# Performance work log

Hardware: AMD Instinct MI355X
Metric: run time of the kernel (lower is better)

Reference implementation:

```python
import jax, jax.numpy as jnp
import numpy as np

B, SEQ, D, H, E = 4, 4096, 1024, 4096, 8
CAPACITY = 2.0  # k = int(S * capacity) token-expert slots


def setup_inputs() -> dict:
    key = jax.random.key(0)
    ks = jax.random.split(key, 5)
    x = jax.random.normal(ks[0], (B, SEQ, D), dtype=jnp.float32)
    gate_weight = jax.random.normal(ks[1], (E, D), dtype=jnp.float32) * 0.006
    expert_bias = jnp.ones((E, 1), dtype=jnp.float32)
    W1 = jax.random.normal(ks[2], (E, D, H), dtype=jnp.float32) * 0.02
    b1 = jnp.zeros((E, H), dtype=jnp.float32)
    W2 = jax.random.normal(ks[3], (E, H, D), dtype=jnp.float32) * 0.02
    b2 = jnp.zeros((E, D), dtype=jnp.float32)
    return {"x": x, "gate_weight": gate_weight, "expert_bias": expert_bias,
            "W1": W1, "b1": b1, "W2": W2, "b2": b2}


def reference(x, gate_weight, expert_bias, W1, b1, W2, b2):
    Bv, s, Dv = x.shape
    xf = x.reshape(-1, Dv)               # [S, D]
    S = xf.shape[0]
    k = int(S * CAPACITY)

    # router: bias_sigmoid -> scores[e, s] = sigmoid(x @ gate.T + bias)
    logits = jnp.einsum('sd,ed->es', xf, gate_weight) + expert_bias  # [E, S]
    scores = jax.nn.sigmoid(logits)

    # global top-k over flattened (E*S) token-expert pairs
    value, index = jax.lax.top_k(scores.reshape(-1), k)
    index_expert = index // S
    index_token = index % S

    # combine weights: gating score at selected slots, 0 elsewhere (topk indices unique)
    C = jnp.zeros((E * S,), dtype=scores.dtype).at[index].set(value).reshape(E, S)

    token_each_expert = jax.ops.segment_sum(
        jnp.ones((k,), dtype=jnp.float32), index_expert, num_segments=E) / float(k)

    # per-expert MLP, gated combine (tokens with C==0 contribute exactly 0,
    # matching the torch gather/MLP/index_add_ path)
    out = jnp.zeros_like(xf)
    for e in range(E):
        h = jax.nn.gelu(xf @ W1[e] + b1[e], approximate=True)  # [S, H]
        y = h @ W2[e] + b2[e]                                  # [S, D]
        out = out + C[e][:, None] * y

    x_out = out.reshape(Bv, s, Dv)
    return x_out, token_each_expert, jnp.ones((E,), dtype=scores.dtype)
```

## Files before the change

kernel.cpp:

```cpp
#include <hip/hip_runtime.h>
#include <hip/hip_bf16.h>
#include <cstdint>
#include <cstdio>
#include <math.h>

#define S_TOK 16384
#define E_EXP 8
#define DDIM  1024
#define HDIM  4096
#define K_SEL 32768
#define ES    131072
#define OUT_XO 16777216

#define WS_META    0x000000u
#define WS_HIST    0x000100u
#define WS_COUNTS  0x001100u
#define WS_EXOFF   0x001200u
#define WS_TIEIDX  0x001300u
#define WS_CLEAR   0x00A000u
#define WS_TOK     0x010000u
#define WS_COEF    0x090000u
#define WS_SCORES  0x110000u
#define WS_TCNT    0x190000u
#define WS_TSLOT   0x1A0000u
#define WS_XB      0x400000u
#define WS_W1T    0x2400000u
#define WS_W2T    0x6400000u
#define WS_HBUF   0xA400000u
#define WS_TOTAL  0x1A400000u
#define WS_YBUF   WS_W1T

typedef __attribute__((ext_vector_type(4))) float f32x4;
typedef __attribute__((ext_vector_type(8))) short bf16x8;

__device__ __forceinline__ void gload_lds16(const void* g, void* l) {
  __builtin_amdgcn_global_load_lds((const __attribute__((address_space(1))) void*)g,
                                   (__attribute__((address_space(3))) void*)l, 16, 0, 0);
}

__device__ __forceinline__ float gelu_f(float x) {
  float u = __builtin_fmaf(x * x * x, 0.044715f, x);
  float e = __builtin_amdgcn_exp2f(-2.302207976f * u);
  return x * __builtin_amdgcn_rcpf(1.0f + e);
}

#define ABUF0 0
#define ABUF1 32768
#define BBUF0 65536
#define BBUF1 98304
#define HALF  16384

#define PH_BAR() __builtin_amdgcn_s_barrier()
#define VMC0M()  asm volatile("s_waitcnt vmcnt(0)" ::: "memory")
#define VMCN(N)  asm volatile("s_waitcnt vmcnt(" #N ")" ::: "memory")

#define STAGE_A(DST, KE) do { \
  gload_lds16(aS00 + (KE), lds + (DST) + w * 2048); \
  gload_lds16(aS01 + (KE), lds + (DST) + w * 2048 + 1024); \
  gload_lds16(aS10 + (KE), lds + (DST) + HALF + w * 2048); \
  gload_lds16(aS11 + (KE), lds + (DST) + HALF + w * 2048 + 1024); } while (0)
#define STAGE_B(DST, KE) do { \
  gload_lds16(bS00 + (KE), lds + (DST) + w * 2048); \
  gload_lds16(bS01 + (KE), lds + (DST) + w * 2048 + 1024); \
  gload_lds16(bS10 + (KE), lds + (DST) + HALF + w * 2048); \
  gload_lds16(bS11 + (KE), lds + (DST) + HALF + w * 2048 + 1024); } while (0)

#define LDS_A03(AB) { _Pragma("unroll") for (int ii = 0; ii < 4; ii++) { \
  a03[ii][0] = *(const bf16x8*)(lds + (AB) + arow + ii * 2048 + pc0); \
  a03[ii][1] = *(const bf16x8*)(lds + (AB) + arow + ii * 2048 + pc1); } }
#define LDS_A47(AB) { _Pragma("unroll") for (int ii = 0; ii < 4; ii++) { \
  a47[ii][0] = *(const bf16x8*)(lds + (AB) + arow + (4 + ii) * 2048 + pc0); \
  a47[ii][1] = *(const bf16x8*)(lds + (AB) + arow + (4 + ii) * 2048 + pc1); } }
#define LDS_B01(BB) { _Pragma("unroll") for (int jj = 0; jj < 2; jj++) { \
  b01[jj][0] = *(const bf16x8*)(lds + (BB) + brow + jj * 2048 + pc0); \
  b01[jj][1] = *(const bf16x8*)(lds + (BB) + brow + jj * 2048 + pc1); } }
#define LDS_B23(BB) { _Pragma("unroll") for (int jj = 0; jj < 2; jj++) { \
  b23[jj][0] = *(const bf16x8*)(lds + (BB) + brow + (2 + jj) * 2048 + pc0); \
  b23[jj][1] = *(const bf16x8*)(lds + (BB) + brow + (2 + jj) * 2048 + pc1); } }

#define MF(AA, BF, IL, JL) { _Pragma("unroll") for (int ii = 0; ii < 4; ii++) \
  _Pragma("unroll") for (int jj = 0; jj < 2; jj++) { \
    acc[(IL)+ii][(JL)+jj] = __builtin_amdgcn_mfma_f32_16x16x32_bf16(AA[ii][0], BF[jj][0], acc[(IL)+ii][(JL)+jj], 0, 0, 0); \
    acc[(IL)+ii][(JL)+jj] = __builtin_amdgcn_mfma_f32_16x16x32_bf16(AA[ii][1], BF[jj][1], acc[(IL)+ii][(JL)+jj], 0, 0, 0); } }

#define TILE(T, AB, BB, ABn, BBn, STGA, STGB, NB, NA) do { \
  PH_BAR(); \
  LDS_A03(AB); \
  if (STGA) STAGE_A(ABn, ((T) + 1) * 64); \
  __builtin_amdgcn_s_setprio(1); MF(a03, b01, 0, 0); MF(a03, b23, 0, 2); __builtin_amdgcn_s_setprio(0); \
  PH_BAR(); \
  LDS_A47(AB); \
  if (STGB) STAGE_B(BB, ((T) + 2) * 64); \
  __builtin_amdgcn_s_setprio(1); MF(a47, b01, 4, 0); __builtin_amdgcn_s_setprio(0); \
  VMCN(NB); \
  LDS_B01(BBn); \
  __builtin_amdgcn_s_setprio(1); MF(a47, b23, 4, 2); __builtin_amdgcn_s_setprio(0); \
  LDS_B23(BBn); \
  VMCN(NA); \
} while (0)

#define TILE_LAST(AB, BB) do { \
  PH_BAR(); \
  LDS_A03(AB); \
  __builtin_amdgcn_s_setprio(1); MF(a03, b01, 0, 0); MF(a03, b23, 0, 2); __builtin_amdgcn_s_setprio(0); \
  PH_BAR(); \
  LDS_A47(AB); \
  __builtin_amdgcn_s_setprio(1); MF(a47, b01, 4, 0); MF(a47, b23, 4, 2); __builtin_amdgcn_s_setprio(0); \
} while (0)

__global__ __launch_bounds__(256) void transpose_bf16_kernel(
    const float* __restrict__ in, __hip_bfloat16* __restrict__ outp, int R, int C)
{
  __shared__ float tile[32][33];
  const int c0 = blockIdx.x * 32, r0 = blockIdx.y * 32;
  const size_t eoff = (size_t)blockIdx.z * (size_t)R * (size_t)C;
  const float* ip = in + eoff;
  __hip_bfloat16* op = outp + eoff;
  const int tx = threadIdx.x, ty = threadIdx.y;
#pragma unroll
  for (int i = 0; i < 4; i++) {
    int r = ty + i * 8;
    tile[r][tx] = ip[(size_t)(r0 + r) * C + c0 + tx];
  }
  __syncthreads();
#pragma unroll
  for (int i = 0; i < 4; i++) {
    int c = ty + i * 8;
    op[(size_t)(c0 + c) * R + r0 + tx] = __float2bfloat16(tile[tx][c]);
  }
}

__global__ __launch_bounds__(256) void router_kernel(
    const float* __restrict__ x, const float* __restrict__ gw, const float* __restrict__ bias,
    float* __restrict__ scores, __hip_bfloat16* __restrict__ xb)
{
  __shared__ float g[E_EXP * DDIM];
  __shared__ float bs[E_EXP];
  const int tid = threadIdx.x;
  for (int i = tid; i < E_EXP * DDIM; i += 256) g[i] = gw[i];
  if (tid < E_EXP) bs[tid] = bias[tid];
  __syncthreads();
  const int w = tid >> 6, lane = tid & 63;
  const int s = blockIdx.x * 4 + w;
  double acc[E_EXP] = {0, 0, 0, 0, 0, 0, 0, 0};
  const float* xrow = x + (size_t)s * DDIM;
  __hip_bfloat16* xbrow = xb + (size_t)s * DDIM;
#pragma unroll 4
  for (int j = 0; j < 16; j++) {
    int d = lane + 64 * j;
    float xv = xrow[d];
    xbrow[d] = __float2bfloat16(xv);
#pragma unroll
    for (int e = 0; e < E_EXP; e++) acc[e] += (double)xv * (double)g[e * DDIM + d];
  }
#pragma unroll
  for (int e = 0; e < E_EXP; e++) {
    double a = acc[e];
#pragma unroll
    for (int off = 32; off > 0; off >>= 1) a += __shfl_xor(a, off);
    acc[e] = a;
  }
  if (lane == 0) {
#pragma unroll
    for (int e = 0; e < E_EXP; e++) {
      double lg = acc[e] + (double)bs[e];
      float sc = (float)(1.0 / (1.0 + exp(-lg)));
      scores[(size_t)e * S_TOK + s] = sc;
    }
  }
}

__global__ __launch_bounds__(256) void hist_pass_kernel(
    const float* __restrict__ scores, const unsigned* __restrict__ meta,
    unsigned* __restrict__ hist, int pass)
{
  __shared__ unsigned h[256];
  const int tid = threadIdx.x;
  h[tid] = 0;
  __syncthreads();
  const unsigned prefix = meta[0];
  const int pshift = 32 - 8 * pass;
  const int bshift = 24 - 8 * pass;
  const unsigned base = blockIdx.x * 2048 + tid;
#pragma unroll
  for (int i = 0; i < 8; i++) {
    unsigned b = __float_as_uint(scores[base + i * 256]);
    bool ok = (pass == 0) || ((b >> pshift) == prefix);
    if (ok) atomicAdd(&h[(b >> bshift) & 0xFFu], 1u);
  }
  __syncthreads();
  if (h[tid]) atomicAdd(&hist[tid], h[tid]);
}

__global__ __launch_bounds__(256) void scan_pass_kernel(
    const unsigned* __restrict__ hist, unsigned* __restrict__ meta, int final)
{
  const int t = threadIdx.x;
  const unsigned v = hist[t];
  const unsigned prefix = meta[0];
  const unsigned above = meta[1];
  __shared__ unsigned csum[256];
  csum[t] = v;
  __syncthreads();
  for (int off = 1; off < 256; off <<= 1) {
    unsigned add = (t + off < 256) ? csum[t + off] : 0u;
    __syncthreads();
    csum[t] += add;
    __syncthreads();
  }
  const unsigned cge = csum[t];
  const unsigned cgt = cge - v;
  if (above + cgt < K_SEL && above + cge >= K_SEL) {
    meta[0] = (prefix << 8) | (unsigned)t;
    meta[1] = above + cgt;
    if (final) {
      meta[2] = (prefix << 8) | (unsigned)t;
      meta[4] = K_SEL - (above + cgt);
    }
  }
}

__global__ __launch_bounds__(256) void sel_kernel(const float* __restrict__ scores,
                                                  unsigned* __restrict__ meta,
                                                  unsigned* __restrict__ counts,
                                                  int* __restrict__ tok_list,
                                                  float* __restrict__ coef_list,
                                                  unsigned* __restrict__ tie_idx,
                                                  unsigned* __restrict__ tcnt,
                                                  unsigned* __restrict__ tslot)
{
  __shared__ unsigned lcnt[E_EXP], lbase[E_EXP];
  const int tid = threadIdx.x;
  if (tid < E_EXP) lcnt[tid] = 0;
  __syncthreads();
  const unsigned i = blockIdx.x * 256 + tid;
  const float v = scores[i];
  const unsigned b = __float_as_uint(v);
  const unsigned t = meta[2];
  const bool sel = (b > t);
  const unsigned e = i >> 14;
  unsigned myslot = 0;
  if (sel) myslot = atomicAdd(&lcnt[e], 1u);
  else if (b == t) {
    unsigned ts = atomicAdd(&meta[5], 1u);
    if (ts < 8192u) tie_idx[ts] = i;
  }
  __syncthreads();
  if (tid < E_EXP) lbase[tid] = atomicAdd(&counts[tid], lcnt[tid]);
  __syncthreads();
  if (sel) {
    const unsigned slot = lbase[e] + myslot;
    const unsigned p = e * S_TOK + slot;
    const unsigned tok = i & 16383u;
    tok_list[p] = (int)tok;
    coef_list[p] = v;
    unsigned us = atomicAdd(&tcnt[tok], 1u);
    tslot[tok * 8u + us] = (e << 14) | slot;
  }
}

__global__ __launch_bounds__(256) void fin_kernel(const unsigned* __restrict__ meta,
                                                  const unsigned* __restrict__ tie_idx,
                                                  unsigned* __restrict__ counts,
                                                  int* __restrict__ tok_list,
                                                  float* __restrict__ coef_list,
                                                  unsigned* __restrict__ tcnt,
                                                  unsigned* __restrict__ tslot)
{
  unsigned tcnt_ties = meta[5]; if (tcnt_ties > 8192u) tcnt_ties = 8192u;
  const unsigned q = meta[4];
  const float tval = __uint_as_float(meta[2]);
  for (unsigned t = threadIdx.x; t < tcnt_ties; t += 256) {
    unsigned idx = tie_idx[t];
    unsigned rank = 0;
    for (unsigned u = 0; u < tcnt_ties; u++) rank += (tie_idx[u] < idx) ? 1u : 0u;
    if (rank < q) {
      const unsigned e = idx >> 14;
      const unsigned tok = idx & 16383u;
      const unsigned slot = atomicAdd(&counts[e], 1u);
      tok_list[e * S_TOK + slot] = (int)tok;
      coef_list[e * S_TOK + slot] = tval;
      unsigned us = atomicAdd(&tcnt[tok], 1u);
      tslot[tok * 8u + us] = (e << 14) | slot;
    }
  }
}

__global__ void tail_kernel(const unsigned* __restrict__ counts, unsigned* __restrict__ exoff,
                            float* __restrict__ tail)
{
  if (threadIdx.x == 0) {
    unsigned o = 0;
    for (int e = 0; e < E_EXP; e++) { exoff[e] = o; o += counts[e]; }
    exoff[E_EXP] = o;
  }
  if (threadIdx.x < E_EXP) {
    tail[threadIdx.x] = (float)counts[threadIdx.x] * (1.0f / (float)K_SEL);
    tail[E_EXP + threadIdx.x] = 1.0f;
  }
}

__global__ __launch_bounds__(512, 1) void gemm1_kernel(
    const __hip_bfloat16* __restrict__ xb,
    const __hip_bfloat16* __restrict__ w1t,
    const float* __restrict__ b1,
    const int* __restrict__ tok_list,
    const unsigned* __restrict__ counts,
    const unsigned* __restrict__ exoff,
    __hip_bfloat16* __restrict__ hbuf)
{
  const int id = blockIdx.x;
  const int L = (id & 7) * 1024 + (id >> 3);
  const int e = L >> 10;
  const int rem = L & 1023;
  const int cnt = (int)counts[e];
  const int m0 = (rem >> 4) * 256;
  if (m0 >= cnt) return;
  const int n0 = (rem & 15) * 256;

  __shared__ __align__(16) char lds[131072];
  __shared__ int s_tok[256];

  const int tid = threadIdx.x;
  const int w = tid >> 6, lane = tid & 63;
  const int wm = w >> 2, wn = w & 3;

  if (tid < 256) {
    int mi = m0 + tid;
    s_tok[tid] = tok_list[e * S_TOK + (mi < cnt ? mi : cnt - 1)];
  }
  __syncthreads();

  const int srl0 = w * 16 + (lane >> 3);
  const int srl1 = srl0 + 8;
  const int gch = ((lane & 7) ^ (lane >> 3)) * 8;
  const __hip_bfloat16* aS00 = xb + (size_t)s_tok[srl0] * DDIM + gch;
  const __hip_bfloat16* aS01 = xb + (size_t)s_tok[srl1] * DDIM + gch;
  const __hip_bfloat16* aS10 = xb + (size_t)s_tok[128 + srl0] * DDIM + gch;
  const __hip_bfloat16* aS11 = xb + (size_t)s_tok[128 + srl1] * DDIM + gch;
  const __hip_bfloat16* w1e = w1t + (size_t)e * HDIM * DDIM;
  const __hip_bfloat16* bS00 = w1e + (size_t)(n0 + srl0) * DDIM + gch;
  const __hip_bfloat16* bS01 = w1e + (size_t)(n0 + srl1) * DDIM + gch;
  const __hip_bfloat16* bS10 = w1e + (size_t)(n0 + 128 + srl0) * DDIM + gch;
  const __hip_bfloat16* bS11 = w1e + (size_t)(n0 + 128 + srl1) * DDIM + gch;

  const int arow = (wm * 128 + (lane & 15)) * 128;
  const int brow = (wn * 64 + (lane & 15)) * 128;
  const int pc0 = (((lane >> 4)) ^ (lane & 7)) * 16;
  const int pc1 = (((lane >> 4) + 4) ^ (lane & 7)) * 16;

  f32x4 acc[8][4] = {};
  bf16x8 a03[4][2], a47[4][2], b01[2][2], b23[2][2];

  STAGE_A(ABUF0, 0);
  STAGE_B(BBUF0, 0);
  STAGE_B(BBUF1, 64);
  VMC0M();
  PH_BAR();
  LDS_B01(BBUF0); LDS_B23(BBUF0);

  const int NKT = DDIM / 64;
  int kt = 0;
  for (; kt + 2 < NKT; kt += 2) {
    TILE(kt,     ABUF0, BBUF0, ABUF1, BBUF1, true, true, 8, 4);
    TILE(kt + 1, ABUF1, BBUF1, ABUF0, BBUF0, true, true, 8, 4);
  }
  TILE(kt, ABUF0, BBUF0, ABUF1, BBUF1, true, false, 4, 0);
  TILE_LAST(ABUF1, BBUF1);
  __syncthreads();

  __hip_bfloat16* stg = (__hip_bfloat16*)lds;
  const float* b1e = b1 + (size_t)e * HDIM;
  float bvj[4];
#pragma unroll
  for (int j = 0; j < 4; j++) bvj[j] = b1e[n0 + wn * 64 + j * 16 + (lane & 15)];
  const int pbase = (int)exoff[e] + m0;

#pragma unroll
  for (int P = 0; P < 4; P++) {
    __syncthreads();
    if (wm == (P >> 1)) {
      const int ib = (P & 1) * 4;
#pragma unroll
      for (int ii = 0; ii < 4; ii++)
#pragma unroll
        for (int jj = 0; jj < 4; jj++)
#pragma unroll
          for (int r = 0; r < 4; r++) {
            const int rloc = ii * 16 + (lane >> 4) * 4 + r;
            const int col = wn * 64 + jj * 16 + (lane & 15);
            stg[rloc * 264 + col] = __float2bfloat16(gelu_f(acc[ib + ii][jj][r] + bvj[jj]));
          }
    }
    __syncthreads();
    const int rr = tid >> 3;
    const int m = P * 64 + rr;
    if (m0 + m < cnt) {
      __hip_bfloat16* dst = hbuf + (size_t)(pbase + m) * HDIM + n0;
      const __hip_bfloat16* src = stg + rr * 264;
#pragma unroll
      for (int c = 0; c < 4; c++)
        *(uint4*)(dst + (tid & 7) * 8 + c * 64) = *(const uint4*)(src + (tid & 7) * 8 + c * 64);
    }
  }
}

__global__ __launch_bounds__(512, 1) void gemm2_kernel(
    const __hip_bfloat16* __restrict__ hbuf,
    const __hip_bfloat16* __restrict__ w2t,
    const float* __restrict__ b2,
    const float* __restrict__ coef_list,
    const unsigned* __restrict__ counts,
    const unsigned* __restrict__ exoff,
    __hip_bfloat16* __restrict__ ybuf)
{
  const int id = blockIdx.x;
  const int L = (id & 7) * 256 + (id >> 3);
  const int e = L >> 8;
  const int rem = L & 255;
  const int cnt = (int)counts[e];
  const int m0 = (rem >> 2) * 256;
  if (m0 >= cnt) return;
  const int n0 = (rem & 3) * 256;

  __shared__ __align__(16) char lds[131072];
  __shared__ float s_coef[256];

  const int tid = threadIdx.x;
  const int w = tid >> 6, lane = tid & 63;
  const int wm = w >> 2, wn = w & 3;
  const int pb = (int)exoff[e];

  if (tid < 256) {
    int mi = m0 + tid;
    s_coef[tid] = (mi < cnt) ? coef_list[e * S_TOK + mi] : 0.0f;
  }
  __syncthreads();

  const int srl0 = w * 16 + (lane >> 3);
  const int srl1 = srl0 + 8;
  const int gch = ((lane & 7) ^ (lane >> 3)) * 8;
  const int ra0 = pb + ((m0 + srl0 < cnt) ? m0 + srl0 : cnt - 1);
  const int ra1 = pb + ((m0 + srl1 < cnt) ? m0 + srl1 : cnt - 1);
  const int ra2 = pb + ((m0 + 128 + srl0 < cnt) ? m0 + 128 + srl0 : cnt - 1);
  const int ra3 = pb + ((m0 + 128 + srl1 < cnt) ? m0 + 128 + srl1 : cnt - 1);
  const __hip_bfloat16* aS00 = hbuf + (size_t)ra0 * HDIM + gch;
  const __hip_bfloat16* aS01 = hbuf + (size_t)ra1 * HDIM + gch;
  const __hip_bfloat16* aS10 = hbuf + (size_t)ra2 * HDIM + gch;
  const __hip_bfloat16* aS11 = hbuf + (size_t)ra3 * HDIM + gch;
  const __hip_bfloat16* w2e = w2t + (size_t)e * DDIM * HDIM;
  const __hip_bfloat16* bS00 = w2e + (size_t)(n0 + srl0) * HDIM + gch;
  const __hip_bfloat16* bS01 = w2e + (size_t)(n0 + srl1) * HDIM + gch;
  const __hip_bfloat16* bS10 = w2e + (size_t)(n0 + 128 + srl0) * HDIM + gch;
  const __hip_bfloat16* bS11 = w2e + (size_t)(n0 + 128 + srl1) * HDIM + gch;

  const int arow = (wm * 128 + (lane & 15)) * 128;
  const int brow = (wn * 64 + (lane & 15)) * 128;
  const int pc0 = (((lane >> 4)) ^ (lane & 7)) * 16;
  const int pc1 = (((lane >> 4) + 4) ^ (lane & 7)) * 16;

  f32x4 acc[8][4] = {};
  bf16x8 a03[4][2], a47[4][2], b01[2][2], b23[2][2];

  STAGE_A(ABUF0, 0);
  STAGE_B(BBUF0, 0);
  STAGE_B(BBUF1, 64);
  VMC0M();
  PH_BAR();
  LDS_B01(BBUF0); LDS_B23(BBUF0);

  const int NKT = HDIM / 64;
  int kt = 0;
  for (; kt + 2 < NKT; kt += 2) {
    TILE(kt,     ABUF0, BBUF0, ABUF1, BBUF1, true, true, 8, 4);
    TILE(kt + 1, ABUF1, BBUF1, ABUF0, BBUF0, true, true, 8, 4);
  }
  TILE(kt, ABUF0, BBUF0, ABUF1, BBUF1, true, false, 4, 0);
  TILE_LAST(ABUF1, BBUF1);
  __syncthreads();

  __hip_bfloat16* stg = (__hip_bfloat16*)lds;
  const float* b2e = b2 + (size_t)e * DDIM;
  float bvj[4];
#pragma unroll
  for (int j = 0; j < 4; j++) bvj[j] = b2e[n0 + wn * 64 + j * 16 + (lane & 15)];
  const int pbase = pb + m0;

#pragma unroll
  for (int P = 0; P < 4; P++) {
    __syncthreads();
    if (wm == (P >> 1)) {
      const int ib = (P & 1) * 4;
#pragma unroll
      for (int ii = 0; ii < 4; ii++)
#pragma unroll
        for (int jj = 0; jj < 4; jj++)
#pragma unroll
          for (int r = 0; r < 4; r++) {
            const int rloc = ii * 16 + (lane >> 4) * 4 + r;
            const int col = wn * 64 + jj * 16 + (lane & 15);
            const float cf = s_coef[P * 64 + rloc];
            stg[rloc * 264 + col] = __float2bfloat16(cf * (acc[ib + ii][jj][r] + bvj[jj]));
          }
    }
    __syncthreads();
    const int rr = tid >> 3;
    const int m = P * 64 + rr;
    if (m0 + m < cnt) {
      __hip_bfloat16* dst = ybuf + (size_t)(pbase + m) * DDIM + n0;
      const __hip_bfloat16* src = stg + rr * 264;
#pragma unroll
      for (int c = 0; c < 4; c++)
        *(uint4*)(dst + (tid & 7) * 8 + c * 64) = *(const uint4*)(src + (tid & 7) * 8 + c * 64);
    }
  }
}

__global__ __launch_bounds__(256) void combine_kernel(
    const __hip_bfloat16* __restrict__ ybuf,
    const unsigned* __restrict__ tcnt,
    const unsigned* __restrict__ tslot,
    const unsigned* __restrict__ exoff,
    float* __restrict__ out)
{
  const int tid = threadIdx.x;
  const int t = blockIdx.x * 2 + (tid >> 7);
  const int d0 = (tid & 127) * 8;
  float a[8] = {0, 0, 0, 0, 0, 0, 0, 0};
  const unsigned n = tcnt[t];
  for (unsigned s = 0; s < n; s++) {
    const unsigned code = tslot[t * 8u + s];
    const unsigned p = exoff[code >> 14] + (code & 16383u);
    bf16x8 v = *(const bf16x8*)(ybuf + (size_t)p * DDIM + d0);
#pragma unroll
    for (int k = 0; k < 8; k++)
      a[k] += __uint_as_float(((unsigned)(unsigned short)v[k]) << 16);
  }
  float* op = out + (size_t)t * DDIM + d0;
  *(float4*)op = make_float4(a[0], a[1], a[2], a[3]);
  *(float4*)(op + 4) = make_float4(a[4], a[5], a[6], a[7]);
}

extern "C" void kernel_launch(void* const* d_in, const int* in_sizes, int n_in,
                              void* d_out, int out_size, void* d_ws, size_t ws_size,
                              hipStream_t stream) {
  const float* x    = (const float*)d_in[0];
  const float* gw   = (const float*)d_in[1];
  const float* bias = (const float*)d_in[2];
  const float* W1   = (const float*)d_in[3];
  const float* b1   = (const float*)d_in[4];
  const float* W2   = (const float*)d_in[5];
  const float* b2   = (const float*)d_in[6];
  float* out = (float*)d_out;
  char* ws = (char*)d_ws;

  if (ws_size < (size_t)WS_TOTAL) {
    fprintf(stderr, "kernel_launch: ws_size %zu < required %u\n", ws_size, WS_TOTAL);
    return;
  }

  unsigned* meta   = (unsigned*)(ws + WS_META);
  unsigned* hist   = (unsigned*)(ws + WS_HIST);
  unsigned* counts = (unsigned*)(ws + WS_COUNTS);
  unsigned* exoff  = (unsigned*)(ws + WS_EXOFF);
  unsigned* tiei   = (unsigned*)(ws + WS_TIEIDX);
  unsigned* tcnt   = (unsigned*)(ws + WS_TCNT);
  unsigned* tslot  = (unsigned*)(ws + WS_TSLOT);
  int*      tokl   = (int*)(ws + WS_TOK);
  float*    coefl  = (float*)(ws + WS_COEF);
  float*    scores = (float*)(ws + WS_SCORES);
  __hip_bfloat16* xb   = (__hip_bfloat16*)(ws + WS_XB);
  __hip_bfloat16* w1t  = (__hip_bfloat16*)(ws + WS_W1T);
  __hip_bfloat16* w2t  = (__hip_bfloat16*)(ws + WS_W2T);
  __hip_bfloat16* hbuf = (__hip_bfloat16*)(ws + WS_HBUF);
  __hip_bfloat16* ybuf = (__hip_bfloat16*)(ws + WS_YBUF);

  hipMemsetAsync(ws, 0, WS_CLEAR, stream);
  hipMemsetAsync(ws + WS_TCNT, 0, S_TOK * sizeof(unsigned), stream);

  transpose_bf16_kernel<<<dim3(HDIM / 32, DDIM / 32, E_EXP), dim3(32, 8), 0, stream>>>(W1, w1t, DDIM, HDIM);
  transpose_bf16_kernel<<<dim3(DDIM / 32, HDIM / 32, E_EXP), dim3(32, 8), 0, stream>>>(W2, w2t, HDIM, DDIM);

  router_kernel<<<S_TOK / 4, 256, 0, stream>>>(x, gw, bias, scores, xb);

  for (int p = 0; p < 4; p++) {
    hist_pass_kernel<<<ES / 2048, 256, 0, stream>>>(scores, meta, hist + p * 256, p);
    scan_pass_kernel<<<1, 256, 0, stream>>>(hist + p * 256, meta, p == 3);
  }
  sel_kernel<<<ES / 256, 256, 0, stream>>>(scores, meta, counts, tokl, coefl, tiei, tcnt, tslot);
  fin_kernel<<<1, 256, 0, stream>>>(meta, tiei, counts, tokl, coefl, tcnt, tslot);
  tail_kernel<<<1, 64, 0, stream>>>(counts, exoff, out + OUT_XO);

  gemm1_kernel<<<8192, 512, 0, stream>>>(xb, w1t, b1, tokl, counts, exoff, hbuf);
  gemm2_kernel<<<2048, 512, 0, stream>>>(hbuf, w2t, b2, coefl, counts, exoff, ybuf);
  combine_kernel<<<S_TOK / 2, 256, 0, stream>>>(ybuf, tcnt, tslot, exoff, out);
}
```

Measured before the change: 860.1 us.

## Switch expert GEMMs to 32x32x16 MFMA with simplified double-buffered pipeline

Both expert GEMM kernels move from 16x16x32 bf16 MFMA fragments to 32x32x16 MFMA, so each wave holds a 4x2 grid of 32x32 accumulators and needs fewer LDS fragment reads per FLOP. The staged pipeline, which prefetched B two tiles ahead with partial vmcnt waits and split barriers, is replaced by a simpler schedule: stage A and B one tile ahead, read four k-slices from LDS, issue MFMAs, then wait vmcnt(0). The epilogue index mapping is rewritten for the 32x32 accumulator layout. The trade is less memory-latency hiding from the simpler pipeline (one barrier per tile and a full vmcnt wait) in exchange for denser MFMA and less LDS traffic.

```diff
diff --git a/kernel.cpp b/kernel.cpp
--- a/kernel.cpp
+++ b/kernel.cpp
@@ -31,6 +31,7 @@
 #define WS_YBUF   WS_W1T
 
 typedef __attribute__((ext_vector_type(4))) float f32x4;
+typedef __attribute__((ext_vector_type(16))) float f32x16;
 typedef __attribute__((ext_vector_type(8))) short bf16x8;
 
 __device__ __forceinline__ void gload_lds16(const void* g, void* l) {
@@ -52,7 +53,6 @@
 
 #define PH_BAR() __builtin_amdgcn_s_barrier()
 #define VMC0M()  asm volatile("s_waitcnt vmcnt(0)" ::: "memory")
-#define VMCN(N)  asm volatile("s_waitcnt vmcnt(" #N ")" ::: "memory")
 
 #define STAGE_A(DST, KE) do { \
   gload_lds16(aS00 + (KE), lds + (DST) + w * 2048); \
@@ -65,47 +65,27 @@
   gload_lds16(bS10 + (KE), lds + (DST) + HALF + w * 2048); \
   gload_lds16(bS11 + (KE), lds + (DST) + HALF + w * 2048 + 1024); } while (0)
 
-#define LDS_A03(AB) { _Pragma("unroll") for (int ii = 0; ii < 4; ii++) { \
-  a03[ii][0] = *(const bf16x8*)(lds + (AB) + arow + ii * 2048 + pc0); \
-  a03[ii][1] = *(const bf16x8*)(lds + (AB) + arow + ii * 2048 + pc1); } }
-#define LDS_A47(AB) { _Pragma("unroll") for (int ii = 0; ii < 4; ii++) { \
-  a47[ii][0] = *(const bf16x8*)(lds + (AB) + arow + (4 + ii) * 2048 + pc0); \
-  a47[ii][1] = *(const bf16x8*)(lds + (AB) + arow + (4 + ii) * 2048 + pc1); } }
-#define LDS_B01(BB) { _Pragma("unroll") for (int jj = 0; jj < 2; jj++) { \
-  b01[jj][0] = *(const bf16x8*)(lds + (BB) + brow + jj * 2048 + pc0); \
-  b01[jj][1] = *(const bf16x8*)(lds + (BB) + brow + jj * 2048 + pc1); } }
-#define LDS_B23(BB) { _Pragma("unroll") for (int jj = 0; jj < 2; jj++) { \
-  b23[jj][0] = *(const bf16x8*)(lds + (BB) + brow + (2 + jj) * 2048 + pc0); \
-  b23[jj][1] = *(const bf16x8*)(lds + (BB) + brow + (2 + jj) * 2048 + pc1); } }
-
-#define MF(AA, BF, IL, JL) { _Pragma("unroll") for (int ii = 0; ii < 4; ii++) \
-  _Pragma("unroll") for (int jj = 0; jj < 2; jj++) { \
-    acc[(IL)+ii][(JL)+jj] = __builtin_amdgcn_mfma_f32_16x16x32_bf16(AA[ii][0], BF[jj][0], acc[(IL)+ii][(JL)+jj], 0, 0, 0); \
-    acc[(IL)+ii][(JL)+jj] = __builtin_amdgcn_mfma_f32_16x16x32_bf16(AA[ii][1], BF[jj][1], acc[(IL)+ii][(JL)+jj], 0, 0, 0); } }
-
-#define TILE(T, AB, BB, ABn, BBn, STGA, STGB, NB, NA) do { \
+#define RDA(KS, AB, DST) { _Pragma("unroll") for (int ii = 0; ii < 4; ii++) \
+  DST[ii] = *(const bf16x8*)(lds + (AB) + aRowB + ii * 4096 + pcc##KS); }
+#define RDB2(KS, BB) { _Pragma("unroll") for (int jj = 0; jj < 2; jj++) \
+  bT##KS[jj] = *(const bf16x8*)(lds + (BB) + bRowB + jj * 4096 + pcc##KS); }
+
+#define MF32(KS, ASET) { _Pragma("unroll") for (int ii = 0; ii < 4; ii++) \
+  _Pragma("unroll") for (int jj = 0; jj < 2; jj++) \
+    acc[ii][jj] = __builtin_amdgcn_mfma_f32_32x32x16_bf16(ASET[ii], bT##KS[jj], acc[ii][jj], 0, 0, 0); }
+
+#define TILE(T, AB, BB, ABn, BBn, STG) do { \
   PH_BAR(); \
-  LDS_A03(AB); \
-  if (STGA) STAGE_A(ABn, ((T) + 1) * 64); \
-  __builtin_amdgcn_s_setprio(1); MF(a03, b01, 0, 0); MF(a03, b23, 0, 2); __builtin_amdgcn_s_setprio(0); \
-  PH_BAR(); \
-  LDS_A47(AB); \
-  if (STGB) STAGE_B(BB, ((T) + 2) * 64); \
-  __builtin_amdgcn_s_setprio(1); MF(a47, b01, 4, 0); __builtin_amdgcn_s_setprio(0); \
-  VMCN(NB); \
-  LDS_B01(BBn); \
-  __builtin_amdgcn_s_setprio(1); MF(a47, b23, 4, 2); __builtin_amdgcn_s_setprio(0); \
-  LDS_B23(BBn); \
-  VMCN(NA); \
-} while (0)
-
-#define TILE_LAST(AB, BB) do { \
-  PH_BAR(); \
-  LDS_A03(AB); \
-  __builtin_amdgcn_s_setprio(1); MF(a03, b01, 0, 0); MF(a03, b23, 0, 2); __builtin_amdgcn_s_setprio(0); \
-  PH_BAR(); \
-  LDS_A47(AB); \
-  __builtin_amdgcn_s_setprio(1); MF(a47, b01, 4, 0); MF(a47, b23, 4, 2); __builtin_amdgcn_s_setprio(0); \
+  if (STG) { STAGE_A(ABn, ((T) + 1) * 64); STAGE_B(BBn, ((T) + 1) * 64); } \
+  RDA(0, AB, aF0); RDB2(0, BB); \
+  RDA(1, AB, aF1); RDB2(1, BB); \
+  __builtin_amdgcn_s_setprio(1); MF32(0, aF0); __builtin_amdgcn_s_setprio(0); \
+  RDA(2, AB, aF0); RDB2(2, BB); \
+  __builtin_amdgcn_s_setprio(1); MF32(1, aF1); __builtin_amdgcn_s_setprio(0); \
+  RDA(3, AB, aF1); RDB2(3, BB); \
+  __builtin_amdgcn_s_setprio(1); MF32(2, aF0); __builtin_amdgcn_s_setprio(0); \
+  __builtin_amdgcn_s_setprio(1); MF32(3, aF1); __builtin_amdgcn_s_setprio(0); \
+  if (STG) VMC0M(); \
 } while (0)
 
 __global__ __launch_bounds__(256) void transpose_bf16_kernel(
@@ -344,52 +324,52 @@
   const __hip_bfloat16* bS10 = w1e + (size_t)(n0 + 128 + srl0) * DDIM + gch;
   const __hip_bfloat16* bS11 = w1e + (size_t)(n0 + 128 + srl1) * DDIM + gch;
 
-  const int arow = (wm * 128 + (lane & 15)) * 128;
-  const int brow = (wn * 64 + (lane & 15)) * 128;
-  const int pc0 = (((lane >> 4)) ^ (lane & 7)) * 16;
-  const int pc1 = (((lane >> 4) + 4) ^ (lane & 7)) * 16;
-
-  f32x4 acc[8][4] = {};
-  bf16x8 a03[4][2], a47[4][2], b01[2][2], b23[2][2];
+  const int aRowB = (wm * 128 + (lane & 31)) * 128;
+  const int bRowB = (wn * 64 + (lane & 31)) * 128;
+  const int g2 = lane >> 5, lx = lane & 7;
+  const int pcc0 = ((0 + g2) ^ lx) * 16;
+  const int pcc1 = ((2 + g2) ^ lx) * 16;
+  const int pcc2 = ((4 + g2) ^ lx) * 16;
+  const int pcc3 = ((6 + g2) ^ lx) * 16;
+
+  f32x16 acc[4][2] = {};
+  bf16x8 aF0[4], aF1[4], bT0[2], bT1[2], bT2[2], bT3[2];
 
   STAGE_A(ABUF0, 0);
   STAGE_B(BBUF0, 0);
-  STAGE_B(BBUF1, 64);
   VMC0M();
-  PH_BAR();
-  LDS_B01(BBUF0); LDS_B23(BBUF0);
 
   const int NKT = DDIM / 64;
   int kt = 0;
-  for (; kt + 2 < NKT; kt += 2) {
-    TILE(kt,     ABUF0, BBUF0, ABUF1, BBUF1, true, true, 8, 4);
-    TILE(kt + 1, ABUF1, BBUF1, ABUF0, BBUF0, true, true, 8, 4);
-  }
-  TILE(kt, ABUF0, BBUF0, ABUF1, BBUF1, true, false, 4, 0);
-  TILE_LAST(ABUF1, BBUF1);
+  for (; kt < NKT - 2; kt += 2) {
+    TILE(kt,     ABUF0, BBUF0, ABUF1, BBUF1, true);
+    TILE(kt + 1, ABUF1, BBUF1, ABUF0, BBUF0, true);
+  }
+  TILE(kt, ABUF0, BBUF0, ABUF1, BBUF1, true);
+  TILE(kt + 1, ABUF1, BBUF1, 0, 0, false);
   __syncthreads();
 
   __hip_bfloat16* stg = (__hip_bfloat16*)lds;
   const float* b1e = b1 + (size_t)e * HDIM;
-  float bvj[4];
-#pragma unroll
-  for (int j = 0; j < 4; j++) bvj[j] = b1e[n0 + wn * 64 + j * 16 + (lane & 15)];
+  float bv[2];
+#pragma unroll
+  for (int jj = 0; jj < 2; jj++) bv[jj] = b1e[n0 + wn * 64 + jj * 32 + (lane & 31)];
   const int pbase = (int)exoff[e] + m0;
 
 #pragma unroll
   for (int P = 0; P < 4; P++) {
     __syncthreads();
     if (wm == (P >> 1)) {
-      const int ib = (P & 1) * 4;
-#pragma unroll
-      for (int ii = 0; ii < 4; ii++)
-#pragma unroll
-        for (int jj = 0; jj < 4; jj++)
-#pragma unroll
-          for (int r = 0; r < 4; r++) {
-            const int rloc = ii * 16 + (lane >> 4) * 4 + r;
-            const int col = wn * 64 + jj * 16 + (lane & 15);
-            stg[rloc * 264 + col] = __float2bfloat16(gelu_f(acc[ib + ii][jj][r] + bvj[jj]));
+      const int iiB = (P & 1) * 2;
+#pragma unroll
+      for (int iq = 0; iq < 2; iq++)
+#pragma unroll
+        for (int jj = 0; jj < 2; jj++)
+#pragma unroll
+          for (int rg = 0; rg < 16; rg++) {
+            const int rloc = iq * 32 + (rg & 3) + 8 * (rg >> 2) + 4 * (lane >> 5);
+            const int col = wn * 64 + jj * 32 + (lane & 31);
+            stg[rloc * 264 + col] = __float2bfloat16(gelu_f(acc[iiB + iq][jj][rg] + bv[jj]));
           }
     }
     __syncthreads();
@@ -454,53 +434,53 @@
   const __hip_bfloat16* bS10 = w2e + (size_t)(n0 + 128 + srl0) * HDIM + gch;
   const __hip_bfloat16* bS11 = w2e + (size_t)(n0 + 128 + srl1) * HDIM + gch;
 
-  const int arow = (wm * 128 + (lane & 15)) * 128;
-  const int brow = (wn * 64 + (lane & 15)) * 128;
-  const int pc0 = (((lane >> 4)) ^ (lane & 7)) * 16;
-  const int pc1 = (((lane >> 4) + 4) ^ (lane & 7)) * 16;
-
-  f32x4 acc[8][4] = {};
-  bf16x8 a03[4][2], a47[4][2], b01[2][2], b23[2][2];
+  const int aRowB = (wm * 128 + (lane & 31)) * 128;
+  const int bRowB = (wn * 64 + (lane & 31)) * 128;
+  const int g2 = lane >> 5, lx = lane & 7;
+  const int pcc0 = ((0 + g2) ^ lx) * 16;
+  const int pcc1 = ((2 + g2) ^ lx) * 16;
+  const int pcc2 = ((4 + g2) ^ lx) * 16;
+  const int pcc3 = ((6 + g2) ^ lx) * 16;
+
+  f32x16 acc[4][2] = {};
+  bf16x8 aF0[4], aF1[4], bT0[2], bT1[2], bT2[2], bT3[2];
 
   STAGE_A(ABUF0, 0);
   STAGE_B(BBUF0, 0);
-  STAGE_B(BBUF1, 64);
   VMC0M();
-  PH_BAR();
-  LDS_B01(BBUF0); LDS_B23(BBUF0);
 
   const int NKT = HDIM / 64;
   int kt = 0;
-  for (; kt + 2 < NKT; kt += 2) {
-    TILE(kt,     ABUF0, BBUF0, ABUF1, BBUF1, true, true, 8, 4);
-    TILE(kt + 1, ABUF1, BBUF1, ABUF0, BBUF0, true, true, 8, 4);
-  }
-  TILE(kt, ABUF0, BBUF0, ABUF1, BBUF1, true, false, 4, 0);
-  TILE_LAST(ABUF1, BBUF1);
+  for (; kt < NKT - 2; kt += 2) {
+    TILE(kt,     ABUF0, BBUF0, ABUF1, BBUF1, true);
+    TILE(kt + 1, ABUF1, BBUF1, ABUF0, BBUF0, true);
+  }
+  TILE(kt, ABUF0, BBUF0, ABUF1, BBUF1, true);
+  TILE(kt + 1, ABUF1, BBUF1, 0, 0, false);
   __syncthreads();
 
   __hip_bfloat16* stg = (__hip_bfloat16*)lds;
   const float* b2e = b2 + (size_t)e * DDIM;
-  float bvj[4];
-#pragma unroll
-  for (int j = 0; j < 4; j++) bvj[j] = b2e[n0 + wn * 64 + j * 16 + (lane & 15)];
+  float bv[2];
+#pragma unroll
+  for (int jj = 0; jj < 2; jj++) bv[jj] = b2e[n0 + wn * 64 + jj * 32 + (lane & 31)];
   const int pbase = pb + m0;
 
 #pragma unroll
   for (int P = 0; P < 4; P++) {
     __syncthreads();
     if (wm == (P >> 1)) {
-      const int ib = (P & 1) * 4;
-#pragma unroll
-      for (int ii = 0; ii < 4; ii++)
-#pragma unroll
-        for (int jj = 0; jj < 4; jj++)
-#pragma unroll
-          for (int r = 0; r < 4; r++) {
-            const int rloc = ii * 16 + (lane >> 4) * 4 + r;
-            const int col = wn * 64 + jj * 16 + (lane & 15);
+      const int iiB = (P & 1) * 2;
+#pragma unroll
+      for (int iq = 0; iq < 2; iq++)
+#pragma unroll
+        for (int jj = 0; jj < 2; jj++)
+#pragma unroll
+          for (int rg = 0; rg < 16; rg++) {
+            const int rloc = iq * 32 + (rg & 3) + 8 * (rg >> 2) + 4 * (lane >> 5);
+            const int col = wn * 64 + jj * 32 + (lane & 31);
             const float cf = s_coef[P * 64 + rloc];
-            stg[rloc * 264 + col] = __float2bfloat16(cf * (acc[ib + ii][jj][r] + bvj[jj]));
+            stg[rloc * 264 + col] = __float2bfloat16(cf * (acc[iiB + iq][jj][rg] + bv[jj]));
           }
     }
     __syncthreads();
```

Result: slower. 971.6 us (+13.0%).

## Vectorize weight transpose, fold first histogram into router, merge tail into fin

Applied to the files above, without the earlier changes.

The weight transpose now uses 64x64 tiles with float4 loads and a bf16 LDS tile, writing ushort4 stores instead of scalar accesses. The router kernel builds the first radix-select histogram in shared memory, which removes the pass-0 histogram kernel. The tail kernel is folded into fin_kernel after a barrier. Together these cut memory traffic in the transpose and remove a few small launches. The costs are extra atomics in the router and LDS bank conflicts on the strided bf16 reads in the transpose.

```diff
diff --git a/kernel.cpp b/kernel.cpp
--- a/kernel.cpp
+++ b/kernel.cpp
@@ -111,34 +111,45 @@
 __global__ __launch_bounds__(256) void transpose_bf16_kernel(
     const float* __restrict__ in, __hip_bfloat16* __restrict__ outp, int R, int C)
 {
-  __shared__ float tile[32][33];
-  const int c0 = blockIdx.x * 32, r0 = blockIdx.y * 32;
+  __shared__ __hip_bfloat16 t[64][66];
+  const int c0 = blockIdx.x * 64, r0 = blockIdx.y * 64;
   const size_t eoff = (size_t)blockIdx.z * (size_t)R * (size_t)C;
-  const float* ip = in + eoff;
-  __hip_bfloat16* op = outp + eoff;
-  const int tx = threadIdx.x, ty = threadIdx.y;
+  const int tx = threadIdx.x & 15, ty = threadIdx.x >> 4;
+  const float* ip = in + eoff + (size_t)r0 * C + c0;
 #pragma unroll
   for (int i = 0; i < 4; i++) {
-    int r = ty + i * 8;
-    tile[r][tx] = ip[(size_t)(r0 + r) * C + c0 + tx];
-  }
-  __syncthreads();
+    const int r = ty + i * 16;
+    float4 v = *(const float4*)(ip + (size_t)r * C + tx * 4);
+    t[r][tx * 4 + 0] = __float2bfloat16(v.x);
+    t[r][tx * 4 + 1] = __float2bfloat16(v.y);
+    t[r][tx * 4 + 2] = __float2bfloat16(v.z);
+    t[r][tx * 4 + 3] = __float2bfloat16(v.w);
+  }
+  __syncthreads();
+  __hip_bfloat16* op = outp + eoff + (size_t)c0 * R + r0;
 #pragma unroll
   for (int i = 0; i < 4; i++) {
-    int c = ty + i * 8;
-    op[(size_t)(c0 + c) * R + r0 + tx] = __float2bfloat16(tile[tx][c]);
+    const int c = ty + i * 16;
+    ushort4 u;
+    u.x = *(const unsigned short*)&t[tx * 4 + 0][c];
+    u.y = *(const unsigned short*)&t[tx * 4 + 1][c];
+    u.z = *(const unsigned short*)&t[tx * 4 + 2][c];
+    u.w = *(const unsigned short*)&t[tx * 4 + 3][c];
+    *(ushort4*)(op + (size_t)c * R + tx * 4) = u;
   }
 }
 
 __global__ __launch_bounds__(256) void router_kernel(
     const float* __restrict__ x, const float* __restrict__ gw, const float* __restrict__ bias,
-    float* __restrict__ scores, __hip_bfloat16* __restrict__ xb)
+    float* __restrict__ scores, __hip_bfloat16* __restrict__ xb, unsigned* __restrict__ hist0)
 {
   __shared__ float g[E_EXP * DDIM];
   __shared__ float bs[E_EXP];
+  __shared__ unsigned h0[256];
   const int tid = threadIdx.x;
   for (int i = tid; i < E_EXP * DDIM; i += 256) g[i] = gw[i];
   if (tid < E_EXP) bs[tid] = bias[tid];
+  h0[tid] = 0;
   __syncthreads();
   const int w = tid >> 6, lane = tid & 63;
   const int s = blockIdx.x * 4 + w;
@@ -166,8 +177,11 @@
       double lg = acc[e] + (double)bs[e];
       float sc = (float)(1.0 / (1.0 + exp(-lg)));
       scores[(size_t)e * S_TOK + s] = sc;
+      atomicAdd(&h0[__float_as_uint(sc) >> 24], 1u);
     }
   }
+  __syncthreads();
+  if (h0[tid]) atomicAdd(&hist0[tid], h0[tid]);
 }
 
 __global__ __launch_bounds__(256) void hist_pass_kernel(
@@ -185,7 +199,7 @@
 #pragma unroll
   for (int i = 0; i < 8; i++) {
     unsigned b = __float_as_uint(scores[base + i * 256]);
-    bool ok = (pass == 0) || ((b >> pshift) == prefix);
+    bool ok = ((b >> pshift) == prefix);
     if (ok) atomicAdd(&h[(b >> bshift) & 0xFFu], 1u);
   }
   __syncthreads();
@@ -265,7 +279,9 @@
                                                   int* __restrict__ tok_list,
                                                   float* __restrict__ coef_list,
                                                   unsigned* __restrict__ tcnt,
-                                                  unsigned* __restrict__ tslot)
+                                                  unsigned* __restrict__ tslot,
+                                                  unsigned* __restrict__ exoff,
+                                                  float* __restrict__ tail)
 {
   unsigned tcnt_ties = meta[5]; if (tcnt_ties > 8192u) tcnt_ties = 8192u;
   const unsigned q = meta[4];
@@ -284,11 +300,7 @@
       tslot[tok * 8u + us] = (e << 14) | slot;
     }
   }
-}
-
-__global__ void tail_kernel(const unsigned* __restrict__ counts, unsigned* __restrict__ exoff,
-                            float* __restrict__ tail)
-{
+  __syncthreads();
   if (threadIdx.x == 0) {
     unsigned o = 0;
     for (int e = 0; e < E_EXP; e++) { exoff[e] = o; o += counts[e]; }
@@ -578,18 +590,18 @@
   hipMemsetAsync(ws, 0, WS_CLEAR, stream);
   hipMemsetAsync(ws + WS_TCNT, 0, S_TOK * sizeof(unsigned), stream);
 
-  transpose_bf16_kernel<<<dim3(HDIM / 32, DDIM / 32, E_EXP), dim3(32, 8), 0, stream>>>(W1, w1t, DDIM, HDIM);
-  transpose_bf16_kernel<<<dim3(DDIM / 32, HDIM / 32, E_EXP), dim3(32, 8), 0, stream>>>(W2, w2t, HDIM, DDIM);
-
-  router_kernel<<<S_TOK / 4, 256, 0, stream>>>(x, gw, bias, scores, xb);
-
-  for (int p = 0; p < 4; p++) {
+  transpose_bf16_kernel<<<dim3(HDIM / 64, DDIM / 64, E_EXP), 256, 0, stream>>>(W1, w1t, DDIM, HDIM);
+  transpose_bf16_kernel<<<dim3(DDIM / 64, HDIM / 64, E_EXP), 256, 0, stream>>>(W2, w2t, HDIM, DDIM);
+
+  router_kernel<<<S_TOK / 4, 256, 0, stream>>>(x, gw, bias, scores, xb, hist);
+
+  scan_pass_kernel<<<1, 256, 0, stream>>>(hist, meta, 0);
+  for (int p = 1; p < 4; p++) {
     hist_pass_kernel<<<ES / 2048, 256, 0, stream>>>(scores, meta, hist + p * 256, p);
     scan_pass_kernel<<<1, 256, 0, stream>>>(hist + p * 256, meta, p == 3);
   }
   sel_kernel<<<ES / 256, 256, 0, stream>>>(scores, meta, counts, tokl, coefl, tiei, tcnt, tslot);
-  fin_kernel<<<1, 256, 0, stream>>>(meta, tiei, counts, tokl, coefl, tcnt, tslot);
-  tail_kernel<<<1, 64, 0, stream>>>(counts, exoff, out + OUT_XO);
+  fin_kernel<<<1, 256, 0, stream>>>(meta, tiei, counts, tokl, coefl, tcnt, tslot, exoff, out + OUT_XO);
 
   gemm1_kernel<<<8192, 512, 0, stream>>>(xb, w1t, b1, tokl, counts, exoff, hbuf);
   gemm2_kernel<<<2048, 512, 0, stream>>>(hbuf, w2t, b2, coefl, counts, exoff, ybuf);
```

Result: no change. 866.0 us, median of 2 (+0.7%).
